# Kernel optimization log

Hardware: AMD Instinct MI355X
Metric: run time of the kernel (lower is better)

The kernel has to match this reference:

```python
import jax, jax.numpy as jnp
import numpy as np
import math

D = 256   # d_model / hidden_size
Q = 256   # q_num (query-side nodes)
K = 512   # k_num (key-side nodes)
NEG = -9e15


def _forward(q_enc, k_enc, rel_k, rel_v, k_adj,
             W_glob, b_glob, W_gv0, b_gv0, W_gv1, b_gv1,
             W_gq, b_gq, W_lq, b_lq,
             W_locgate, b_locgate, W_gate, b_gate):
    d = q_enc.shape[-1]
    scale = 1.0 / math.sqrt(d)
    act = jnp.tanh  # activation_func='tanh'

    # --- global sigmoid blending of k_enc with the mean query encoding ---
    q_glob_enc = jnp.mean(q_enc, axis=0)                       # [d]
    k_s = jax.nn.sigmoid((q_glob_enc @ W_glob + b_glob) @ k_enc.T * scale)  # [K]
    k_s = k_s[:, None]                                         # [K,1]
    g_1 = q_glob_enc @ W_gv0 + b_gv0                           # [d]
    k_1 = k_enc @ W_gv1 + b_gv1                                # [K,d]
    k_enc2 = (1.0 - k_s) * k_1 + k_s * g_1                     # [K,d]

    # --- global relation-aware attention over k nodes ---
    q_glob = q_enc @ W_gq + b_gq                               # [Q,d]
    qk_logit = q_glob @ k_enc2.T                               # [Q,K]
    qk_r = jnp.einsum('qd,qkd->qk', q_glob, rel_k)             # [Q,K]
    glob_attn = jax.nn.softmax(act((qk_logit + qk_r) * scale), axis=-1)  # [Q,K]

    # --- local adjacency-masked attention ---
    q_loc = q_enc @ W_lq + b_lq                                # [Q,d]
    qnk_logit = q_loc @ k_enc2.T                               # [Q,K]
    qnk_r = jnp.einsum('qd,qkd->qk', q_loc, rel_k)             # [Q,K]
    loc_attn = act((qnk_logit + qnk_r) * scale)                # [Q,K]
    # loc_weight_rep[q,i,j] = loc_attn[q,j]  (repeat + view in torch)
    mask = (k_adj != 0)[None, :, :]                            # [1,K,K]
    masked = jnp.where(mask, loc_attn[:, None, :], NEG)        # [Q,K,K]
    attn_adj_norm = jax.nn.softmax(masked, axis=-1)            # [Q,K,K]
    k_loc = jnp.einsum('qij,jd->qid', attn_adj_norm, k_enc2)   # [Q,K,d]

    # --- local gate between neighborhood value and self value ---
    # sigmoid(cat([k_loc, k_self]) @ W_locgate + b); k_self is broadcast k_enc2
    Wg1, Wg2 = W_locgate[:d], W_locgate[d:]                    # [d,1] each
    gate_logit = (jnp.einsum('qid,d->qi', k_loc, Wg1[:, 0])
                  + (k_enc2 @ Wg2)[None, :, 0] + b_locgate[0])  # [Q,K]
    loc_gate = jax.nn.sigmoid(gate_logit)[..., None]           # [Q,K,1]
    k_awr = loc_gate * k_loc + (1.0 - loc_gate) * k_enc2[None, :, :]  # [Q,K,d]

    # --- aggregate with global attention + relation values ---
    k_matmul = jnp.einsum('qk,qkd->qd', glob_attn, k_awr)      # [Q,d]
    k_r_matmul = jnp.einsum('qk,qkd->qd', glob_attn, rel_v)    # [Q,d]
    q_enc_new = k_matmul + k_r_matmul                          # [Q,d]

    # --- residual gate ---
    Wq1, Wq2 = W_gate[:d], W_gate[d:]
    gate = jax.nn.sigmoid(q_enc_new @ Wq1 + q_enc @ Wq2 + b_gate)  # [Q,1]
    h = gate * q_enc_new + (1.0 - gate) * q_enc                # [Q,d]
    return h


def setup_inputs() -> dict:
    key = jax.random.key(0)
    ks = jax.random.split(key, 16)
    def w(k, shape):
        return jax.random.normal(k, shape, jnp.float32) * 0.02
    return {
        'q_enc': jax.random.normal(ks[0], (Q, D), jnp.float32),
        'k_enc': jax.random.normal(ks[1], (K, D), jnp.float32),
        'rel_k': jax.random.normal(ks[2], (Q, K, D), jnp.float32) * 0.1,
        'rel_v': jax.random.normal(ks[3], (Q, K, D), jnp.float32) * 0.1,
        'k_adj': jax.random.randint(ks[4], (K, K), 0, 2, jnp.int64) if jax.config.jax_enable_x64 else jax.random.randint(ks[4], (K, K), 0, 2, jnp.int32),
        'W_glob': w(ks[5], (D, D)), 'b_glob': jnp.zeros((D,), jnp.float32),
        'W_gv0': w(ks[6], (D, D)), 'b_gv0': jnp.zeros((D,), jnp.float32),
        'W_gv1': w(ks[7], (D, D)), 'b_gv1': jnp.zeros((D,), jnp.float32),
        'W_gq': w(ks[8], (D, D)), 'b_gq': jnp.zeros((D,), jnp.float32),
        'W_lq': w(ks[9], (D, D)), 'b_lq': jnp.zeros((D,), jnp.float32),
        'W_locgate': w(ks[10], (2 * D, 1)), 'b_locgate': jnp.zeros((1,), jnp.float32),
        'W_gate': w(ks[11], (2 * D, 1)), 'b_gate': jnp.zeros((1,), jnp.float32),
    }


def reference(q_enc, k_enc, rel_k, rel_v, k_adj,
              W_glob, b_glob, W_gv0, b_gv0, W_gv1, b_gv1,
              W_gq, b_gq, W_lq, b_lq,
              W_locgate, b_locgate, W_gate, b_gate):
    return _forward(q_enc, k_enc, rel_k, rel_v, k_adj,
                    W_glob, b_glob, W_gv0, b_gv0, W_gv1, b_gv1,
                    W_gq, b_gq, W_lq, b_lq,
                    W_locgate, b_locgate, W_gate, b_gate)
```

## Files before the change

### kernel.cpp

```cpp
#include <hip/hip_runtime.h>
#include <math.h>

#define QN 256
#define KN 512
#define DN 256
#define SCALE 0.0625f

typedef __attribute__((ext_vector_type(8))) short short8v;
typedef __attribute__((ext_vector_type(4))) float f32x4;

__device__ __forceinline__ float sigf(float x){ return 1.0f/(1.0f+expf(-x)); }

__device__ __forceinline__ unsigned short f2bf(float x){
  unsigned u = __float_as_uint(x);
  unsigned r = (u + 0x7FFFu + ((u >> 16) & 1u)) >> 16;
  return (unsigned short)r;
}

__device__ __forceinline__ short8v ld8(const unsigned short* p){
  ushort4 a = *(const ushort4*)p;
  ushort4 b = *(const ushort4*)(p + 16);
  short8v r;
  r[0]=(short)a.x; r[1]=(short)a.y; r[2]=(short)a.z; r[3]=(short)a.w;
  r[4]=(short)b.x; r[5]=(short)b.y; r[6]=(short)b.z; r[7]=(short)b.w;
  return r;
}

__device__ __forceinline__ float wave_red(float v){
  #pragma unroll
  for (int off = 32; off; off >>= 1) v += __shfl_down(v, off);
  return v;
}

__global__ void kA2(const float* __restrict__ q_enc,
                    const float* __restrict__ W_glob, const float* __restrict__ W_gv0,
                    float* __restrict__ party0, float* __restrict__ party1,
                    const int* __restrict__ kadj, unsigned short* __restrict__ mbf){
  __shared__ float sm[256][9];
  __shared__ float qm[8];
  int b = blockIdx.x, t = threadIdx.x;
  int j0 = b*8;
  #pragma unroll
  for (int i = 0; i < 8; ++i){
    int gi = b*2048 + i*256 + t;
    int4 v = ((const int4*)kadj)[gi];
    ushort4 o;
    o.x = v.x ? 0x3F80 : 0; o.y = v.y ? 0x3F80 : 0;
    o.z = v.z ? 0x3F80 : 0; o.w = v.w ? 0x3F80 : 0;
    ((ushort4*)mbf)[gi] = o;
  }
  float4 lo = *(const float4*)(q_enc + (size_t)t*DN + j0);
  float4 hi = *(const float4*)(q_enc + (size_t)t*DN + j0 + 4);
  sm[t][0]=lo.x; sm[t][1]=lo.y; sm[t][2]=lo.z; sm[t][3]=lo.w;
  sm[t][4]=hi.x; sm[t][5]=hi.y; sm[t][6]=hi.z; sm[t][7]=hi.w;
  __syncthreads();
  #pragma unroll
  for (int s = 128; s > 0; s >>= 1){
    if (t < s){
      #pragma unroll
      for (int j = 0; j < 8; ++j) sm[t][j] += sm[t+s][j];
    }
    __syncthreads();
  }
  if (t < 8) qm[t] = sm[0][t] * (1.0f/QN);
  __syncthreads();
  float a0 = 0.f, a1 = 0.f;
  #pragma unroll
  for (int j = 0; j < 8; ++j){
    float s = qm[j];
    a0 = fmaf(s, W_glob[(size_t)(j0+j)*DN + t], a0);
    a1 = fmaf(s, W_gv0[(size_t)(j0+j)*DN + t], a1);
  }
  party0[b*256 + t] = a0; party1[b*256 + t] = a1;
}

__global__ void k23(const float* __restrict__ k_enc,
                    const float* __restrict__ W_gv1, const float* __restrict__ b_gv1,
                    const float* __restrict__ party0, const float* __restrict__ party1,
                    const float* __restrict__ b_glob, const float* __restrict__ b_gv0,
                    const float* __restrict__ W_locgate,
                    float* __restrict__ k_enc2, float* __restrict__ cvec,
                    float* __restrict__ gl2,
                    const float* __restrict__ q_enc,
                    const float* __restrict__ W_gq, const float* __restrict__ b_gq,
                    const float* __restrict__ W_lq, const float* __restrict__ b_lq,
                    float* __restrict__ q_glob, float* __restrict__ q_loc){
  __shared__ float sh1[256];
  __shared__ float red8[8];
  int bid = blockIdx.x, t = threadIdx.x;
  int w = t >> 6, lane = t & 63;
  if (bid < 512){
    int k = bid;
    float tg = b_glob[t], g1v = b_gv0[t];
    #pragma unroll 8
    for (int b2 = 0; b2 < 32; ++b2){
      tg  += party0[b2*256 + t];
      g1v += party1[b2*256 + t];
    }
    float kv = k_enc[(size_t)k*DN + t];
    sh1[t] = kv;
    float part = wave_red(kv * tg);
    if (lane == 0) red8[w] = part;
    __syncthreads();
    float dot = red8[0] + red8[1] + red8[2] + red8[3];
    float ks = sigf(dot * SCALE);
    float acc = b_gv1[t];
    #pragma unroll 8
    for (int j = 0; j < DN; ++j) acc = fmaf(sh1[j], W_gv1[(size_t)j*DN + t], acc);
    float v = (1.f - ks)*acc + ks*g1v;
    k_enc2[(size_t)k*DN + t] = v;
    float pc = wave_red(v * W_locgate[t]);
    float pg = wave_red(v * W_locgate[DN + t]);
    __syncthreads();
    if (lane == 0){ red8[w] = pc; red8[4 + w] = pg; }
    __syncthreads();
    if (t == 0) cvec[k] = red8[0] + red8[1] + red8[2] + red8[3];
    if (t == 1) gl2[k]  = red8[4] + red8[5] + red8[6] + red8[7];
  } else {
    int q = bid - 512;
    sh1[t] = q_enc[(size_t)q*DN + t];
    __syncthreads();
    float a = b_gq[t], b = b_lq[t];
    #pragma unroll 8
    for (int j = 0; j < DN; ++j){
      float s = sh1[j];
      a = fmaf(s, W_gq[(size_t)j*DN + t], a);
      b = fmaf(s, W_lq[(size_t)j*DN + t], b);
    }
    q_glob[(size_t)q*DN + t] = a; q_loc[(size_t)q*DN + t] = b;
  }
}

__global__ __launch_bounds__(256) void kbf(const float* __restrict__ rel_k,
                    const float* __restrict__ rel_v,
                    const float* __restrict__ q_glob, const float* __restrict__ q_loc,
                    const float* __restrict__ ke2, const float* __restrict__ cvec,
                    float* __restrict__ exs,
                    unsigned short* __restrict__ ebf, unsigned short* __restrict__ ecbf,
                    float* __restrict__ part){
  __shared__ f32x4 sacc[4][16][4];
  int t = threadIdx.x;
  int wv = t >> 6, lane = t & 63;
  int g = lane >> 4, l16 = lane & 15;
  int b = blockIdx.x;
  int q = b >> 3, slice = b & 7;
  int base = lane & 48;
  float4 a4[4], b4[4];
  #pragma unroll
  for (int it = 0; it < 4; ++it){
    int d = it*64 + l16*4;
    a4[it] = *(const float4*)(q_glob + (size_t)q*DN + d);
    b4[it] = *(const float4*)(q_loc  + (size_t)q*DN + d);
  }
  f32x4 racc[4];
  #pragma unroll
  for (int it = 0; it < 4; ++it) racc[it] = (f32x4){0.f,0.f,0.f,0.f};

  int k = slice*64 + wv*4 + g;
  size_t ro = ((size_t)q*KN + k)*DN;
  f32x4 x[4], y[4];
  #pragma unroll
  for (int it = 0; it < 4; ++it){
    int d = it*64 + l16*4;
    x[it] = *(const f32x4*)(rel_k + ro + d);
    y[it] = *(const f32x4*)(rel_v + ro + d);
  }
  #pragma unroll
  for (int kq = 0; kq < 4; ++kq){
    f32x4 xn[4], yn[4];
    if (kq < 3){
      size_t ro2 = ((size_t)q*KN + (k + 16))*DN;
      #pragma unroll
      for (int it = 0; it < 4; ++it){
        int d = it*64 + l16*4;
        xn[it] = *(const f32x4*)(rel_k + ro2 + d);
        yn[it] = *(const f32x4*)(rel_v + ro2 + d);
      }
    }
    float p1 = 0.f, p2 = 0.f, p3 = 0.f, p4 = 0.f;
    #pragma unroll
    for (int it = 0; it < 4; ++it){
      int d = it*64 + l16*4;
      float4 c = *(const float4*)(ke2 + (size_t)k*DN + d);
      float4 a = a4[it], bb = b4[it];
      p1 += x[it][0]*a.x  + x[it][1]*a.y  + x[it][2]*a.z  + x[it][3]*a.w;
      p2 += x[it][0]*bb.x + x[it][1]*bb.y + x[it][2]*bb.z + x[it][3]*bb.w;
      p3 += c.x*a.x  + c.y*a.y  + c.z*a.z  + c.w*a.w;
      p4 += c.x*bb.x + c.y*bb.y + c.z*bb.z + c.w*bb.w;
    }
    #pragma unroll
    for (int off = 8; off; off >>= 1){
      p1 += __shfl_down(p1, off); p2 += __shfl_down(p2, off);
      p3 += __shfl_down(p3, off); p4 += __shfl_down(p4, off);
    }
    float p13 = __shfl(p1 + p3, base);
    float p24 = __shfl(p2 + p4, base);
    float exv = expf(tanhf(p13*SCALE));
    float evv = expf(tanhf(p24*SCALE));
    if (l16 == 0){
      size_t idx = (size_t)q*KN + k;
      exs[idx] = exv;
      ebf[idx] = f2bf(evv);
      ecbf[idx] = f2bf(evv * cvec[k]);
    }
    #pragma unroll
    for (int it = 0; it < 4; ++it){
      racc[it][0] = fmaf(exv, y[it][0], racc[it][0]);
      racc[it][1] = fmaf(exv, y[it][1], racc[it][1]);
      racc[it][2] = fmaf(exv, y[it][2], racc[it][2]);
      racc[it][3] = fmaf(exv, y[it][3], racc[it][3]);
    }
    if (kq < 3){
      #pragma unroll
      for (int it = 0; it < 4; ++it){ x[it] = xn[it]; y[it] = yn[it]; }
      k += 16;
    }
  }
  #pragma unroll
  for (int h = 16; h <= 32; h <<= 1){
    #pragma unroll
    for (int it = 0; it < 4; ++it){
      racc[it][0] += __shfl_xor(racc[it][0], h);
      racc[it][1] += __shfl_xor(racc[it][1], h);
      racc[it][2] += __shfl_xor(racc[it][2], h);
      racc[it][3] += __shfl_xor(racc[it][3], h);
    }
  }
  if (lane < 16){
    #pragma unroll
    for (int it = 0; it < 4; ++it) sacc[wv][lane][it] = racc[it];
  }
  __syncthreads();
  if (t < 64){
    int it = t >> 4, lb = t & 15;
    f32x4 r0 = sacc[0][lb][it], r1 = sacc[1][lb][it];
    f32x4 r2 = sacc[2][lb][it], r3 = sacc[3][lb][it];
    f32x4 r = r0 + r1 + r2 + r3;
    int d = it*64 + lb*4;
    *(f32x4*)(part + ((size_t)slice*QN + q)*DN + d) = r;
  }
}

__global__ __launch_bounds__(256) void kcA2m(const unsigned short* __restrict__ ebf,
                                             const unsigned short* __restrict__ ecbf,
                                             const unsigned short* __restrict__ mbf,
                                             const float* __restrict__ exs,
                                             const float* __restrict__ gl2,
                                             const float* __restrict__ blg_p,
                                             unsigned short* __restrict__ wvbf,
                                             float* __restrict__ v2){
  __shared__ unsigned short Ae[16*520];
  __shared__ unsigned short Ac[16*520];
  __shared__ unsigned short Bm[64*520];
  int t = threadIdx.x;
  int i0 = blockIdx.x*64, q0 = blockIdx.y*16;
  #pragma unroll
  for (int it = 0; it < 4; ++it){
    int c = t + 256*it; int row = c >> 6, col = (c & 63)*8;
    *(uint4*)&Ae[row*520 + col] = *(const uint4*)&ebf[(size_t)(q0+row)*KN + col];
    *(uint4*)&Ac[row*520 + col] = *(const uint4*)&ecbf[(size_t)(q0+row)*KN + col];
  }
  #pragma unroll
  for (int it = 0; it < 16; ++it){
    int c = t + 256*it; int row = c >> 6, col = (c & 63)*8;
    *(uint4*)&Bm[row*520 + col] = *(const uint4*)&mbf[(size_t)(i0+row)*KN + col];
  }
  __syncthreads();
  int w = t >> 6, l = t & 63;
  int g16 = l >> 4, l16 = l & 15;
  f32x4 aS = {0.f,0.f,0.f,0.f}, aN = {0.f,0.f,0.f,0.f};
  const unsigned short* pe = &Ae[l16*520];
  const unsigned short* pc = &Ac[l16*520];
  const unsigned short* pb = &Bm[(16*w + l16)*520];
  #pragma unroll
  for (int kk = 0; kk < 16; ++kk){
    int k0 = kk*32 + 4*g16;
    short8v fa = ld8(pe + k0);
    short8v fc = ld8(pc + k0);
    short8v fb = ld8(pb + k0);
    aS = __builtin_amdgcn_mfma_f32_16x16x32_bf16(fa, fb, aS, 0, 0, 0);
    aN = __builtin_amdgcn_mfma_f32_16x16x32_bf16(fc, fb, aN, 0, 0, 0);
  }
  float blg = blg_p[0];
  int i = i0 + 16*w + l16;
  float gli = gl2[i];
  #pragma unroll
  for (int r = 0; r < 4; ++r){
    int q = q0 + 4*g16 + r;
    size_t idx = (size_t)q*KN + i;
    float s = aS[r], n = aN[r];
    float lgv = sigf(n/s + gli + blg);
    float ex = exs[idx];
    wvbf[idx] = f2bf(ex*lgv/s);
    v2[idx] = ex*(1.f - lgv);
  }
}

__global__ __launch_bounds__(1024) void kE3(const float* __restrict__ ke2,
                                            const float* __restrict__ exs,
                                            const unsigned short* __restrict__ wvbf,
                                            const unsigned short* __restrict__ mbf,
                                            const unsigned short* __restrict__ ebf,
                                            const float* __restrict__ v2,
                                            const float* __restrict__ part,
                                            const float* __restrict__ q_enc,
                                            const float* __restrict__ W_gate,
                                            const float* __restrict__ b_gate,
                                            float* __restrict__ out){
  __shared__ float red[512];
  __shared__ float wvs[512];
  __shared__ float sacc[4][512];
  __shared__ float coefs[512];
  __shared__ float4 pacc[16][64];
  int q = blockIdx.x, t = threadIdx.x, w = t >> 6, lane = t & 63;
  if (t < 512){
    red[t] = exs[(size_t)q*KN + t];
    wvs[t] = __uint_as_float(((unsigned)wvbf[(size_t)q*KN + t]) << 16);
  }
  __syncthreads();
  #pragma unroll
  for (int s = 256; s > 0; s >>= 1){
    if (t < s) red[t] += red[t+s];
    __syncthreads();
  }
  float invs = 1.0f / red[0];
  {
    int tq = t & 255, ti = t >> 8;
    int j0 = tq*2;
    float a0 = 0.f, a1 = 0.f;
    int ibase = ti*128;
    #pragma unroll 8
    for (int ii = 0; ii < 128; ++ii){
      int i = ibase + ii;
      unsigned mm = *(const unsigned*)(mbf + (size_t)i*KN + j0);
      float wvi = wvs[i];
      a0 = fmaf(wvi, __uint_as_float((mm & 0xFFFFu) << 16), a0);
      a1 = fmaf(wvi, __uint_as_float((mm >> 16) << 16), a1);
    }
    sacc[ti][j0] = a0; sacc[ti][j0+1] = a1;
  }
  __syncthreads();
  if (t < 512){
    float u = sacc[0][t] + sacc[1][t] + sacc[2][t] + sacc[3][t];
    float evv = __uint_as_float(((unsigned)ebf[(size_t)q*KN + t]) << 16);
    coefs[t] = u*evv + v2[(size_t)q*KN + t];
  }
  __syncthreads();
  float4 acc;
  if ((w & 1) == 0){
    f32x4 pv = *(const f32x4*)(part + ((size_t)(w >> 1)*QN + q)*DN + lane*4);
    acc = make_float4(pv[0], pv[1], pv[2], pv[3]);
  } else {
    acc = make_float4(0.f, 0.f, 0.f, 0.f);
  }
  int kbase = w*32;
  #pragma unroll 8
  for (int kk = 0; kk < 32; ++kk){
    int k = kbase + kk;
    float ck = coefs[k];
    float4 kv = ((const float4*)(ke2 + (size_t)k*DN))[lane];
    acc.x = fmaf(ck, kv.x, acc.x);
    acc.y = fmaf(ck, kv.y, acc.y);
    acc.z = fmaf(ck, kv.z, acc.z);
    acc.w = fmaf(ck, kv.w, acc.w);
  }
  pacc[w][lane] = acc;
  __syncthreads();
  if (t < 64){
    float4 r = pacc[0][t];
    #pragma unroll
    for (int w2 = 1; w2 < 16; ++w2){
      float4 p = pacc[w2][t];
      r.x += p.x; r.y += p.y; r.z += p.z; r.w += p.w;
    }
    r.x *= invs; r.y *= invs; r.z *= invs; r.w *= invs;
    float4 qe = ((const float4*)(q_enc + (size_t)q*DN))[t];
    float4 w1 = ((const float4*)(W_gate))[t];
    float4 w2v = ((const float4*)(W_gate + DN))[t];
    float pd = r.x*w1.x + r.y*w1.y + r.z*w1.z + r.w*w1.w
             + qe.x*w2v.x + qe.y*w2v.y + qe.z*w2v.z + qe.w*w2v.w;
    #pragma unroll
    for (int off = 32; off; off >>= 1) pd += __shfl_down(pd, off);
    float gate = sigf(__shfl(pd, 0) + b_gate[0]);
    float4 h;
    h.x = gate*r.x + (1.f-gate)*qe.x;
    h.y = gate*r.y + (1.f-gate)*qe.y;
    h.z = gate*r.z + (1.f-gate)*qe.z;
    h.w = gate*r.w + (1.f-gate)*qe.w;
    ((float4*)(out + (size_t)q*DN))[t] = h;
  }
}

extern "C" void kernel_launch(void* const* d_in, const int* in_sizes, int n_in,
                              void* d_out, int out_size, void* d_ws, size_t ws_size,
                              hipStream_t stream){
  const float* q_enc     = (const float*)d_in[0];
  const float* k_enc     = (const float*)d_in[1];
  const float* rel_k     = (const float*)d_in[2];
  const float* rel_v     = (const float*)d_in[3];
  const int*   k_adj     = (const int*)  d_in[4];
  const float* W_glob    = (const float*)d_in[5];
  const float* b_glob    = (const float*)d_in[6];
  const float* W_gv0     = (const float*)d_in[7];
  const float* b_gv0     = (const float*)d_in[8];
  const float* W_gv1     = (const float*)d_in[9];
  const float* b_gv1     = (const float*)d_in[10];
  const float* W_gq      = (const float*)d_in[11];
  const float* b_gq      = (const float*)d_in[12];
  const float* W_lq      = (const float*)d_in[13];
  const float* b_lq      = (const float*)d_in[14];
  const float* W_locgate = (const float*)d_in[15];
  const float* b_locgate = (const float*)d_in[16];
  const float* W_gate    = (const float*)d_in[17];
  const float* b_gate    = (const float*)d_in[18];
  float* out = (float*)d_out;

  float* ws = (float*)d_ws;
  float* party0   = ws;
  float* party1   = party0 + 8192;
  float* k_enc2   = party1 + 8192;
  float* cvec     = k_enc2 + 131072;
  float* gl2      = cvec + 512;
  float* q_glob   = gl2 + 512;
  float* q_loc    = q_glob + 65536;
  float* exs      = q_loc + 65536;
  float* v2       = exs + 131072;
  float* part     = v2 + 131072;
  unsigned short* mbf  = (unsigned short*)(part + 524288);
  unsigned short* ebf  = mbf + 262144;
  unsigned short* ecbf = ebf + 131072;
  unsigned short* wvbf = ecbf + 131072;

  kA2<<<32, 256, 0, stream>>>(q_enc, W_glob, W_gv0, party0, party1, k_adj, mbf);
  k23<<<768, 256, 0, stream>>>(k_enc, W_gv1, b_gv1, party0, party1, b_glob, b_gv0,
                               W_locgate, k_enc2, cvec, gl2,
                               q_enc, W_gq, b_gq, W_lq, b_lq, q_glob, q_loc);
  kbf<<<2048, 256, 0, stream>>>(rel_k, rel_v, q_glob, q_loc, k_enc2, cvec,
                                exs, ebf, ecbf, part);
  kcA2m<<<dim3(8, 16), 256, 0, stream>>>(ebf, ecbf, mbf, exs, gl2, b_locgate, wvbf, v2);
  kE3<<<256, 1024, 0, stream>>>(k_enc2, exs, wvbf, mbf, ebf, v2, part,
                                q_enc, W_gate, b_gate, out);
}
```

Baseline: 86.81 us.

## Stage rel_v in LDS as bf16 and decouple exp computation from value accumulation

The kbf kernel no longer keeps rel_v rows in registers with manual software prefetch. It now converts each rel_v row to bf16 and stores it in shared memory while the dot products are computed. The dot products are merged into two sums by adding ke2 to rel_k first. Exponentials are then computed once per key by 64 threads, and a separate phase accumulates the exp-weighted values from LDS and reduces them across quarters. The aim is lower register pressure and fewer shuffles, at the cost of extra barriers, LDS traffic and bf16 rounding of rel_v.

```diff
diff --git a/kernel.cpp b/kernel.cpp
--- a/kernel.cpp
+++ b/kernel.cpp
@@ -15,6 +15,10 @@
   unsigned u = __float_as_uint(x);
   unsigned r = (u + 0x7FFFu + ((u >> 16) & 1u)) >> 16;
   return (unsigned short)r;
+}
+
+__device__ __forceinline__ float bfdec(unsigned v){
+  return __uint_as_float(v << 16);
 }
 
 __device__ __forceinline__ short8v ld8(const unsigned short* p){
@@ -138,13 +142,15 @@
                     float* __restrict__ exs,
                     unsigned short* __restrict__ ebf, unsigned short* __restrict__ ecbf,
                     float* __restrict__ part){
-  __shared__ f32x4 sacc[4][16][4];
+  __shared__ unsigned short y_lds[64*264];
+  __shared__ float2 p_lds[64];
+  __shared__ float  ex_s[64];
+  __shared__ f32x4  pacc[4][64];
   int t = threadIdx.x;
   int wv = t >> 6, lane = t & 63;
   int g = lane >> 4, l16 = lane & 15;
   int b = blockIdx.x;
   int q = b >> 3, slice = b & 7;
-  int base = lane & 48;
   float4 a4[4], b4[4];
   #pragma unroll
   for (int it = 0; it < 4; ++it){
@@ -152,92 +158,70 @@
     a4[it] = *(const float4*)(q_glob + (size_t)q*DN + d);
     b4[it] = *(const float4*)(q_loc  + (size_t)q*DN + d);
   }
-  f32x4 racc[4];
-  #pragma unroll
-  for (int it = 0; it < 4; ++it) racc[it] = (f32x4){0.f,0.f,0.f,0.f};
-
-  int k = slice*64 + wv*4 + g;
-  size_t ro = ((size_t)q*KN + k)*DN;
-  f32x4 x[4], y[4];
-  #pragma unroll
-  for (int it = 0; it < 4; ++it){
-    int d = it*64 + l16*4;
-    x[it] = *(const f32x4*)(rel_k + ro + d);
-    y[it] = *(const f32x4*)(rel_v + ro + d);
-  }
   #pragma unroll
   for (int kq = 0; kq < 4; ++kq){
-    f32x4 xn[4], yn[4];
-    if (kq < 3){
-      size_t ro2 = ((size_t)q*KN + (k + 16))*DN;
-      #pragma unroll
-      for (int it = 0; it < 4; ++it){
-        int d = it*64 + l16*4;
-        xn[it] = *(const f32x4*)(rel_k + ro2 + d);
-        yn[it] = *(const f32x4*)(rel_v + ro2 + d);
-      }
-    }
-    float p1 = 0.f, p2 = 0.f, p3 = 0.f, p4 = 0.f;
+    int kl = kq*16 + wv*4 + g;
+    int k  = slice*64 + kl;
+    size_t ro = ((size_t)q*KN + k)*DN;
+    float p13 = 0.f, p24 = 0.f;
     #pragma unroll
     for (int it = 0; it < 4; ++it){
       int d = it*64 + l16*4;
+      f32x4 x = *(const f32x4*)(rel_k + ro + d);
+      f32x4 y = *(const f32x4*)(rel_v + ro + d);
       float4 c = *(const float4*)(ke2 + (size_t)k*DN + d);
       float4 a = a4[it], bb = b4[it];
-      p1 += x[it][0]*a.x  + x[it][1]*a.y  + x[it][2]*a.z  + x[it][3]*a.w;
-      p2 += x[it][0]*bb.x + x[it][1]*bb.y + x[it][2]*bb.z + x[it][3]*bb.w;
-      p3 += c.x*a.x  + c.y*a.y  + c.z*a.z  + c.w*a.w;
-      p4 += c.x*bb.x + c.y*bb.y + c.z*bb.z + c.w*bb.w;
+      p13 += (x[0]+c.x)*a.x  + (x[1]+c.y)*a.y  + (x[2]+c.z)*a.z  + (x[3]+c.w)*a.w;
+      p24 += (x[0]+c.x)*bb.x + (x[1]+c.y)*bb.y + (x[2]+c.z)*bb.z + (x[3]+c.w)*bb.w;
+      unsigned lo, hi;
+      asm("v_cvt_pk_bf16_f32 %0, %1, %2" : "=v"(lo) : "v"(y[0]), "v"(y[1]));
+      asm("v_cvt_pk_bf16_f32 %0, %1, %2" : "=v"(hi) : "v"(y[2]), "v"(y[3]));
+      *(uint2*)&y_lds[kl*264 + d] = make_uint2(lo, hi);
     }
     #pragma unroll
     for (int off = 8; off; off >>= 1){
-      p1 += __shfl_down(p1, off); p2 += __shfl_down(p2, off);
-      p3 += __shfl_down(p3, off); p4 += __shfl_down(p4, off);
-    }
-    float p13 = __shfl(p1 + p3, base);
-    float p24 = __shfl(p2 + p4, base);
-    float exv = expf(tanhf(p13*SCALE));
-    float evv = expf(tanhf(p24*SCALE));
-    if (l16 == 0){
-      size_t idx = (size_t)q*KN + k;
-      exs[idx] = exv;
-      ebf[idx] = f2bf(evv);
-      ecbf[idx] = f2bf(evv * cvec[k]);
-    }
-    #pragma unroll
-    for (int it = 0; it < 4; ++it){
-      racc[it][0] = fmaf(exv, y[it][0], racc[it][0]);
-      racc[it][1] = fmaf(exv, y[it][1], racc[it][1]);
-      racc[it][2] = fmaf(exv, y[it][2], racc[it][2]);
-      racc[it][3] = fmaf(exv, y[it][3], racc[it][3]);
-    }
-    if (kq < 3){
-      #pragma unroll
-      for (int it = 0; it < 4; ++it){ x[it] = xn[it]; y[it] = yn[it]; }
-      k += 16;
-    }
-  }
-  #pragma unroll
-  for (int h = 16; h <= 32; h <<= 1){
-    #pragma unroll
-    for (int it = 0; it < 4; ++it){
-      racc[it][0] += __shfl_xor(racc[it][0], h);
-      racc[it][1] += __shfl_xor(racc[it][1], h);
-      racc[it][2] += __shfl_xor(racc[it][2], h);
-      racc[it][3] += __shfl_xor(racc[it][3], h);
-    }
-  }
-  if (lane < 16){
-    #pragma unroll
-    for (int it = 0; it < 4; ++it) sacc[wv][lane][it] = racc[it];
+      p13 += __shfl_down(p13, off);
+      p24 += __shfl_down(p24, off);
+    }
+    if (l16 == 0) p_lds[kl] = make_float2(p13, p24);
   }
   __syncthreads();
   if (t < 64){
-    int it = t >> 4, lb = t & 15;
-    f32x4 r0 = sacc[0][lb][it], r1 = sacc[1][lb][it];
-    f32x4 r2 = sacc[2][lb][it], r3 = sacc[3][lb][it];
-    f32x4 r = r0 + r1 + r2 + r3;
-    int d = it*64 + lb*4;
-    *(f32x4*)(part + ((size_t)slice*QN + q)*DN + d) = r;
+    int k = slice*64 + t;
+    float2 p = p_lds[t];
+    float exv = expf(tanhf(p.x*SCALE));
+    float evv = expf(tanhf(p.y*SCALE));
+    size_t idx = (size_t)q*KN + k;
+    exs[idx] = exv;
+    ebf[idx] = f2bf(evv);
+    ecbf[idx] = f2bf(evv * cvec[k]);
+    ex_s[t] = exv;
+  }
+  __syncthreads();
+  {
+    int chunk = t & 63, quarter = t >> 6;
+    f32x4 r = {0.f, 0.f, 0.f, 0.f};
+    #pragma unroll 4
+    for (int i = 0; i < 16; ++i){
+      int kk = quarter*16 + i;
+      uint2 yy = *(const uint2*)&y_lds[kk*264 + chunk*4];
+      float e = ex_s[kk];
+      r[0] = fmaf(e, bfdec(yy.x & 0xFFFFu), r[0]);
+      r[1] = fmaf(e, bfdec(yy.x >> 16),     r[1]);
+      r[2] = fmaf(e, bfdec(yy.y & 0xFFFFu), r[2]);
+      r[3] = fmaf(e, bfdec(yy.y >> 16),     r[3]);
+    }
+    pacc[quarter][chunk] = r;
+  }
+  __syncthreads();
+  if (t < 64){
+    f32x4 r = pacc[0][t];
+    f32x4 r1 = pacc[1][t], r2 = pacc[2][t], r3 = pacc[3][t];
+    r[0] += r1[0] + r2[0] + r3[0];
+    r[1] += r1[1] + r2[1] + r3[1];
+    r[2] += r1[2] + r2[2] + r3[2];
+    r[3] += r1[3] + r2[3] + r3[3];
+    *(f32x4*)(part + ((size_t)slice*QN + q)*DN + t*4) = r;
   }
 }
 
```

New measurement: 84.77 us (median of 2 runs). 2.4% less time.
